# Optimization experiments

Hardware: AMD Instinct MI355X
Metric: run time of the kernel (lower is better)

## Reference

```python
import jax, jax.numpy as jnp
import numpy as np

N = 8192
D = 1024
TAU = 1.0
ALPHA = 1.0
BETA = 0.0


def setup_inputs() -> dict:
    key = jax.random.key(0)
    z = jax.random.normal(key, (2 * N, D), dtype=jnp.float32)
    return {"z": z}


def reference(z):
    n = z.shape[0] // 2
    x1, x2 = z[:n], z[n:]
    x1_abs = jnp.linalg.norm(x1, axis=1)  # [N]
    x2_abs = jnp.linalg.norm(x2, axis=1)  # [N]
    # cosine similarity matrix / tau: [N, N]
    matrix = jnp.einsum('ik,jk->ij', x1, x2) / (x1_abs[:, None] * x2_abs[None, :]) / TAU
    pos_sim = jnp.diagonal(matrix)                     # [N]
    neg_sim = (matrix.sum(axis=1) - pos_sim) / (n - 1)  # [N]
    sim_matrix = jnp.exp(matrix)
    pos = jnp.diagonal(sim_matrix)
    p_ij = pos / (sim_matrix.sum(axis=1) - pos)
    alpha = jax.lax.stop_gradient(p_ij - 1.0 + ALPHA)
    loss = -jnp.log(p_ij) - alpha * pos_sim + neg_sim * BETA
    return (loss.mean(), p_ij.mean())
```

## Files before the change

### kernel.cpp

```cpp
#include <hip/hip_runtime.h>
#include <hip/hip_bf16.h>

typedef __hip_bfloat16 bf16_t;
typedef __attribute__((ext_vector_type(8))) short  s16x8;
typedef __attribute__((ext_vector_type(4))) float  f32x4;

#define N_ROWS 8192
#define D_DIM  1024

#define GLOAD_LDS16(g, l)                                                     \
  __builtin_amdgcn_global_load_lds(                                           \
      (const __attribute__((address_space(1))) void*)(g),                     \
      (__attribute__((address_space(3))) void*)(l), 16, 0, 0)

#define WAITCNT_VM(n) asm volatile("s_waitcnt vmcnt(" #n ")" ::: "memory")

struct alignas(8) bf16x4_s { bf16_t x, y, z, w; };

__global__ void __launch_bounds__(256) normalize_kernel(
    const float* __restrict__ z, bf16_t* __restrict__ out,
    float* __restrict__ rowsum) {
  const int row = blockIdx.x;
  const int t   = threadIdx.x;
  if (row < 32) rowsum[row * 256 + t] = 0.f;
  const float4 v = ((const float4*)(z + (size_t)row * D_DIM))[t];
  float ss = v.x * v.x + v.y * v.y + v.z * v.z + v.w * v.w;
  for (int off = 32; off; off >>= 1) ss += __shfl_down(ss, off);
  __shared__ float wss[4];
  const int wv = t >> 6, ln = t & 63;
  if (ln == 0) wss[wv] = ss;
  __syncthreads();
  const float rn = rsqrtf(wss[0] + wss[1] + wss[2] + wss[3]);
  bf16x4_s o;
  o.x = __float2bfloat16(v.x * rn);
  o.y = __float2bfloat16(v.y * rn);
  o.z = __float2bfloat16(v.z * rn);
  o.w = __float2bfloat16(v.w * rn);
  ((bf16x4_s*)(out + (size_t)row * D_DIM))[t] = o;
}

__global__ void __launch_bounds__(512, 2) simexp_gemm(
    const bf16_t* __restrict__ A, const bf16_t* __restrict__ B,
    float* __restrict__ rowsum, float* __restrict__ pos_sim) {
  constexpr int BK   = 32;
  constexpr int ABUF = 256 * BK;
  constexpr int BUFE = 2 * ABUF;
  __shared__ bf16_t lds[3 * BUFE];

  const int t    = threadIdx.x;
  const int w    = t >> 6;
  const int lane = t & 63;
  const int wr   = w >> 2;
  const int wc   = w & 3;
  const int rb   = blockIdx.y, cb = blockIdx.x;
  const int row0 = rb * 256, col0 = cb * 256;

  const int srow = t >> 2;
  const int scol = (((t & 3) ^ ((t >> 3) & 3))) * 8;
  const size_t gA0 = (size_t)(row0 + srow) * D_DIM + scol;
  const size_t gA1 = gA0 + (size_t)128 * D_DIM;
  const size_t gB0 = (size_t)(col0 + srow) * D_DIM + scol;
  const size_t gB1 = gB0 + (size_t)128 * D_DIM;
  const int ldst = w * 512;

#define STAGE_A(dst, k0)                                        \
  do {                                                          \
    GLOAD_LDS16(A + gA0 + (k0), (dst) + ldst);                  \
    GLOAD_LDS16(A + gA1 + (k0), (dst) + 4096 + ldst);           \
  } while (0)
#define STAGE_B(dst, k0)                                        \
  do {                                                          \
    GLOAD_LDS16(B + gB0 + (k0), (dst) + ABUF + ldst);           \
    GLOAD_LDS16(B + gB1 + (k0), (dst) + ABUF + 4096 + ldst);    \
  } while (0)

  int offA[8], offB[4];
#pragma unroll
  for (int m = 0; m < 8; ++m) {
    const int r = wr * 128 + m * 16 + (lane & 15);
    offA[m] = r * 32 + (((lane >> 4) ^ ((r >> 1) & 3)) * 8);
  }
#pragma unroll
  for (int n = 0; n < 4; ++n) {
    const int r = wc * 64 + n * 16 + (lane & 15);
    offB[n] = r * 32 + (((lane >> 4) ^ ((r >> 1) & 3)) * 8);
  }

  f32x4 acc[8][4];
#pragma unroll
  for (int m = 0; m < 8; ++m)
#pragma unroll
    for (int n = 0; n < 4; ++n) acc[m][n] = (f32x4){0.f, 0.f, 0.f, 0.f};

  bf16_t* b0 = lds;
  bf16_t* b1 = lds + BUFE;
  bf16_t* b2 = lds + 2 * BUFE;

  STAGE_A(b0, 0); STAGE_B(b0, 0);
  STAGE_A(b1, BK); STAGE_B(b1, BK);
  WAITCNT_VM(4);
  __builtin_amdgcn_s_barrier();

#pragma unroll 1
  for (int kt = 0; kt < 32; ++kt) {
    const int k0n = (kt + 2) * BK;
    const bf16_t* Ab = b0;
    const bf16_t* Bb = b0 + ABUF;

    if (kt < 30) STAGE_A(b2, k0n);
    s16x8 bf[4];
#pragma unroll
    for (int n = 0; n < 4; ++n) bf[n] = *(const s16x8*)&Bb[offB[n]];
    s16x8 af[4];
#pragma unroll
    for (int m = 0; m < 4; ++m) af[m] = *(const s16x8*)&Ab[offA[m]];
    __builtin_amdgcn_s_setprio(1);
#pragma unroll
    for (int m = 0; m < 4; ++m)
#pragma unroll
      for (int n = 0; n < 4; ++n)
        acc[m][n] = __builtin_amdgcn_mfma_f32_16x16x32_bf16(
            af[m], bf[n], acc[m][n], 0, 0, 0);
    __builtin_amdgcn_s_setprio(0);

    if (kt < 30) STAGE_B(b2, k0n);
#pragma unroll
    for (int m = 0; m < 4; ++m) af[m] = *(const s16x8*)&Ab[offA[m + 4]];
    __builtin_amdgcn_s_setprio(1);
#pragma unroll
    for (int m = 0; m < 4; ++m)
#pragma unroll
      for (int n = 0; n < 4; ++n)
        acc[m + 4][n] = __builtin_amdgcn_mfma_f32_16x16x32_bf16(
            af[m], bf[n], acc[m + 4][n], 0, 0, 0);
    __builtin_amdgcn_s_setprio(0);

    if (kt < 30) {
      WAITCNT_VM(4);
      __builtin_amdgcn_s_barrier();
    } else if (kt == 30) {
      WAITCNT_VM(0);
      __builtin_amdgcn_s_barrier();
    }
    bf16_t* tmp = b0; b0 = b1; b1 = b2; b2 = tmp;
  }

  if (rb == cb) {
#pragma unroll
    for (int m = 0; m < 8; ++m)
#pragma unroll
      for (int n = 0; n < 4; ++n)
#pragma unroll
        for (int r = 0; r < 4; ++r) {
          const int grow = wr * 128 + m * 16 + (lane >> 4) * 4 + r;
          const int gcol = wc * 64 + n * 16 + (lane & 15);
          if (grow == gcol) pos_sim[row0 + grow] = acc[m][n][r];
        }
  }

  __syncthreads();
  float* red = (float*)lds;
#pragma unroll
  for (int m = 0; m < 8; ++m)
#pragma unroll
    for (int r = 0; r < 4; ++r) {
      float s = 0.f;
#pragma unroll
      for (int n = 0; n < 4; ++n) s += __expf(acc[m][n][r]);
      s += __shfl_xor(s, 1);
      s += __shfl_xor(s, 2);
      s += __shfl_xor(s, 4);
      s += __shfl_xor(s, 8);
      if ((lane & 15) == 0) {
        const int row_local = wr * 128 + m * 16 + (lane >> 4) * 4 + r;
        red[wc * 256 + row_local] = s;
      }
    }
  __syncthreads();
  if (t < 256) {
    const float s4 = red[t] + red[256 + t] + red[512 + t] + red[768 + t];
    atomicAdd(&rowsum[row0 + t], s4);
  }
#undef STAGE_A
#undef STAGE_B
}

__global__ void __launch_bounds__(256) finalize_kernel(
    const float* __restrict__ rowsum, const float* __restrict__ pos_sim,
    float* __restrict__ out) {
  const int t = threadIdx.x;
  double lsum = 0.0, psum = 0.0;
  for (int i = t; i < N_ROWS; i += 256) {
    const float ps    = pos_sim[i];
    const float pos   = expf(ps);
    const float denom = rowsum[i] - pos;
    const float p     = pos / denom;
    lsum += (double)(-logf(p) - p * ps);
    psum += (double)p;
  }
  for (int off = 32; off; off >>= 1) {
    lsum += __shfl_down(lsum, off);
    psum += __shfl_down(psum, off);
  }
  __shared__ double sl[4], sp[4];
  const int wv = t >> 6, ln = t & 63;
  if (ln == 0) { sl[wv] = lsum; sp[wv] = psum; }
  __syncthreads();
  if (t == 0) {
    const double L = sl[0] + sl[1] + sl[2] + sl[3];
    const double P = sp[0] + sp[1] + sp[2] + sp[3];
    out[0] = (float)(L / N_ROWS);
    out[1] = (float)(P / N_ROWS);
  }
}

extern "C" void kernel_launch(void* const* d_in, const int* in_sizes, int n_in,
                              void* d_out, int out_size, void* d_ws,
                              size_t ws_size, hipStream_t stream) {
  const float* z = (const float*)d_in[0];
  float* out = (float*)d_out;

  char* ws = (char*)d_ws;
  bf16_t* AB = (bf16_t*)ws;
  float* rowsum  = (float*)(ws + (size_t)2 * N_ROWS * D_DIM * sizeof(bf16_t));
  float* pos_sim = rowsum + N_ROWS;

  normalize_kernel<<<2 * N_ROWS, 256, 0, stream>>>(z, AB, rowsum);

  bf16_t* Amat = AB;
  bf16_t* Bmat = AB + (size_t)N_ROWS * D_DIM;
  dim3 grid(N_ROWS / 256, N_ROWS / 256);
  simexp_gemm<<<grid, 512, 0, stream>>>(Amat, Bmat, rowsum, pos_sim);

  finalize_kernel<<<1, 256, 0, stream>>>(rowsum, pos_sim, out);
}
```

Before: 240.7 us.

## Deepen GEMM LDS pipeline to four stages and process one row per wave in normalize

The similarity GEMM moves from a triple-buffered to a quadruple-buffered LDS ring with a prefetch distance of three K-tiles, with waitcnt thresholds adjusted to match. This hides more global-load latency, at the cost of more LDS per block. The normalize kernel now assigns one row per wavefront and reduces with xor shuffles, which removes the shared-memory reduction and block barrier and cuts the block count by four.

```diff
diff --git a/kernel.cpp b/kernel.cpp
--- a/kernel.cpp
+++ b/kernel.cpp
@@ -20,23 +20,35 @@
 __global__ void __launch_bounds__(256) normalize_kernel(
     const float* __restrict__ z, bf16_t* __restrict__ out,
     float* __restrict__ rowsum) {
-  const int row = blockIdx.x;
-  const int t   = threadIdx.x;
-  if (row < 32) rowsum[row * 256 + t] = 0.f;
-  const float4 v = ((const float4*)(z + (size_t)row * D_DIM))[t];
-  float ss = v.x * v.x + v.y * v.y + v.z * v.z + v.w * v.w;
-  for (int off = 32; off; off >>= 1) ss += __shfl_down(ss, off);
-  __shared__ float wss[4];
-  const int wv = t >> 6, ln = t & 63;
-  if (ln == 0) wss[wv] = ss;
-  __syncthreads();
-  const float rn = rsqrtf(wss[0] + wss[1] + wss[2] + wss[3]);
-  bf16x4_s o;
-  o.x = __float2bfloat16(v.x * rn);
-  o.y = __float2bfloat16(v.y * rn);
-  o.z = __float2bfloat16(v.z * rn);
-  o.w = __float2bfloat16(v.w * rn);
-  ((bf16x4_s*)(out + (size_t)row * D_DIM))[t] = o;
+  const int t = threadIdx.x;
+  if (blockIdx.x < 32) rowsum[blockIdx.x * 256 + t] = 0.f;
+  const int row  = blockIdx.x * 4 + (t >> 6);
+  const int lane = t & 63;
+  const float4* rp = (const float4*)(z + (size_t)row * D_DIM);
+  float4 v[4];
+#pragma unroll
+  for (int j = 0; j < 4; ++j) v[j] = rp[lane + 64 * j];
+  float ss = 0.f;
+#pragma unroll
+  for (int j = 0; j < 4; ++j)
+    ss += v[j].x * v[j].x + v[j].y * v[j].y + v[j].z * v[j].z + v[j].w * v[j].w;
+  ss += __shfl_xor(ss, 1);
+  ss += __shfl_xor(ss, 2);
+  ss += __shfl_xor(ss, 4);
+  ss += __shfl_xor(ss, 8);
+  ss += __shfl_xor(ss, 16);
+  ss += __shfl_xor(ss, 32);
+  const float rn = rsqrtf(ss);
+  bf16x4_s* op = (bf16x4_s*)(out + (size_t)row * D_DIM);
+#pragma unroll
+  for (int j = 0; j < 4; ++j) {
+    bf16x4_s o;
+    o.x = __float2bfloat16(v[j].x * rn);
+    o.y = __float2bfloat16(v[j].y * rn);
+    o.z = __float2bfloat16(v[j].z * rn);
+    o.w = __float2bfloat16(v[j].w * rn);
+    op[lane + 64 * j] = o;
+  }
 }
 
 __global__ void __launch_bounds__(512, 2) simexp_gemm(
@@ -45,7 +57,7 @@
   constexpr int BK   = 32;
   constexpr int ABUF = 256 * BK;
   constexpr int BUFE = 2 * ABUF;
-  __shared__ bf16_t lds[3 * BUFE];
+  __shared__ bf16_t lds[4 * BUFE];
 
   const int t    = threadIdx.x;
   const int w    = t >> 6;
@@ -92,22 +104,20 @@
 #pragma unroll
     for (int n = 0; n < 4; ++n) acc[m][n] = (f32x4){0.f, 0.f, 0.f, 0.f};
 
-  bf16_t* b0 = lds;
-  bf16_t* b1 = lds + BUFE;
-  bf16_t* b2 = lds + 2 * BUFE;
-
-  STAGE_A(b0, 0); STAGE_B(b0, 0);
-  STAGE_A(b1, BK); STAGE_B(b1, BK);
-  WAITCNT_VM(4);
+  STAGE_A(lds, 0);                 STAGE_B(lds, 0);
+  STAGE_A(lds + BUFE, BK);         STAGE_B(lds + BUFE, BK);
+  STAGE_A(lds + 2 * BUFE, 2 * BK); STAGE_B(lds + 2 * BUFE, 2 * BK);
+  WAITCNT_VM(8);
   __builtin_amdgcn_s_barrier();
 
 #pragma unroll 1
   for (int kt = 0; kt < 32; ++kt) {
-    const int k0n = (kt + 2) * BK;
-    const bf16_t* Ab = b0;
-    const bf16_t* Bb = b0 + ABUF;
-
-    if (kt < 30) STAGE_A(b2, k0n);
+    const int k0n = (kt + 3) * BK;
+    const bf16_t* Ab = lds + (kt & 3) * BUFE;
+    const bf16_t* Bb = Ab + ABUF;
+    bf16_t* nxt = lds + ((kt + 3) & 3) * BUFE;
+
+    if (kt < 29) STAGE_A(nxt, k0n);
     s16x8 bf[4];
 #pragma unroll
     for (int n = 0; n < 4; ++n) bf[n] = *(const s16x8*)&Bb[offB[n]];
@@ -123,7 +133,7 @@
             af[m], bf[n], acc[m][n], 0, 0, 0);
     __builtin_amdgcn_s_setprio(0);
 
-    if (kt < 30) STAGE_B(b2, k0n);
+    if (kt < 29) STAGE_B(nxt, k0n);
 #pragma unroll
     for (int m = 0; m < 4; ++m) af[m] = *(const s16x8*)&Ab[offA[m + 4]];
     __builtin_amdgcn_s_setprio(1);
@@ -135,14 +145,16 @@
             af[m], bf[n], acc[m + 4][n], 0, 0, 0);
     __builtin_amdgcn_s_setprio(0);
 
-    if (kt < 30) {
+    if (kt < 29) {
+      WAITCNT_VM(8);
+      __builtin_amdgcn_s_barrier();
+    } else if (kt == 29) {
       WAITCNT_VM(4);
       __builtin_amdgcn_s_barrier();
     } else if (kt == 30) {
       WAITCNT_VM(0);
       __builtin_amdgcn_s_barrier();
     }
-    bf16_t* tmp = b0; b0 = b1; b1 = b2; b2 = tmp;
   }
 
   if (rb == cb) {
@@ -225,7 +237,7 @@
   float* rowsum  = (float*)(ws + (size_t)2 * N_ROWS * D_DIM * sizeof(bf16_t));
   float* pos_sim = rowsum + N_ROWS;
 
-  normalize_kernel<<<2 * N_ROWS, 256, 0, stream>>>(z, AB, rowsum);
+  normalize_kernel<<<2 * N_ROWS / 4, 256, 0, stream>>>(z, AB, rowsum);
 
   bf16_t* Amat = AB;
   bf16_t* Bmat = AB + (size_t)N_ROWS * D_DIM;
```

After: 246.4 us. +2.4%, slower.
